# Kernel tuning notes

Hardware: AMD Instinct MI355X
Metric: run time of the kernel (lower is better)

## Reference

```python
import jax, jax.numpy as jnp
import numpy as np

B, IN, ED, PW, OUT, CL, NK = 2048, 4096, 8192, 2048, 256, 16, 32
MIX = 0.5

def _onehot_mask(key, n):
    # near-one-hot selector matrix [n, NK], as built by forward_update_masks
    idx = jax.random.choice(key, n, (NK,), replace=False)
    return jnp.zeros((n, NK), jnp.float32).at[idx, jnp.arange(NK)].set(1.0)

def setup_inputs():
    ks = jax.random.split(jax.random.key(0), 24)
    f = jnp.float32
    adj = (jax.random.uniform(ks[4], (IN, IN)) < 0.01).astype(f)
    adj = jnp.maximum(adj, adj.T).at[jnp.arange(IN), jnp.arange(IN)].set(1.0)
    return {
        'x_gene': jax.random.normal(ks[0], (B, IN), f),
        'x_invmea': jax.random.normal(ks[1], (B, IN), f),
        'x_curv': jax.random.normal(ks[2], (B, ED), f),
        'clinn': jax.random.normal(ks[3], (B, CL), f),
        'Adj': adj,
        'edge_mask': (jax.random.uniform(ks[5], (ED, IN)) < 0.005).astype(f),
        'pathway_mask': (jax.random.uniform(ks[6], (PW, ED)) < 0.02).astype(f),
        'top_gene_mask': _onehot_mask(ks[7], IN),
        'top_invmea_mask': _onehot_mask(ks[8], IN),
        'top_curv_mask': _onehot_mask(ks[9], ED),
        'top_path_mask': _onehot_mask(ks[10], PW),
        'W1': jnp.full((IN, IN), 0.05, f),
        'b1': 0.01 * jax.random.normal(ks[11], (IN,), f),
        'W2': jnp.full((ED, IN), 0.05, f),
        'b2': 0.01 * jax.random.normal(ks[12], (ED,), f),
        'W3': jnp.full((PW, ED), 0.05, f),
        'b3': 0.01 * jax.random.normal(ks[13], (PW,), f),
        'W4': 0.02 * jax.random.normal(ks[14], (OUT, PW), f),
        'b4': 0.01 * jax.random.normal(ks[15], (OUT,), f),
        'W5': 0.02 * jax.random.normal(ks[16], (OUT, OUT), f),
        'b5': 0.01 * jax.random.normal(ks[17], (OUT,), f),
        'W6': 0.05 * jax.random.normal(ks[18], (OUT, OUT + CL + 4 * NK), f),
        'W7': 0.05 * jax.random.normal(ks[19], (1, OUT), f),
        'mp11': MIX * jnp.ones(IN, f),
        'mp12': (1.0 - MIX) * jnp.ones(IN, f),
        'mp1': jnp.ones(IN, f),
        'mp21': MIX * jnp.ones(ED, f),
        'mp22': (1.0 - MIX) * jnp.ones(ED, f),
        'mp2': jnp.ones(ED, f),
        'mp3': jnp.ones(PW, f),
    }

def reference(x_gene, x_invmea, x_curv, clinn, Adj, edge_mask, pathway_mask,
              top_gene_mask, top_invmea_mask, top_curv_mask, top_path_mask,
              W1, b1, W2, b2, W3, b3, W4, b4, W5, b5, W6, W7,
              mp11, mp12, mp1, mp21, mp22, mp2, mp3):
    sg = jax.lax.stop_gradient
    sig = jax.nn.sigmoid
    kept_gene = sg(x_gene @ top_gene_mask)                     # [B,NK] gather-as-matmul
    x1 = sig(x_gene @ (W1 * Adj).T + b1)                       # masked linear [B,IN]
    x1 = x_invmea * (mp11 * mp1) + x1 * (mp12 * mp1)
    kept_invmea = sg(x1 @ top_invmea_mask)
    x1 = sig(x1 @ (W2 * edge_mask).T + b2)                     # [B,ED]
    x1 = x_curv * (mp21 * mp2) + x1 * (mp22 * mp2)
    kept_curv = sg(x1 @ top_curv_mask)
    x1 = sig(x1 @ (W3 * pathway_mask).T + b3)                  # [B,PW]
    x1 = x1 * mp3
    kept_path = sg(x1 @ top_path_mask)
    x1 = sig(x1 @ W4.T + b4)
    x1 = sig(x1 @ W5.T + b5)                                   # [B,OUT]
    x_cat = jnp.concatenate([x1, kept_gene, kept_invmea, kept_curv, kept_path, clinn], axis=1)
    lp = sig(x_cat @ W6.T)
    lp = lp - jnp.mean(lp, axis=1, keepdims=True)
    return lp @ W7.T                                           # [B,1]
```

## Files before the change

### kernel.cpp

```cpp
#include <hip/hip_runtime.h>

typedef unsigned short u16;
typedef __attribute__((ext_vector_type(4))) float f32x4;
typedef __attribute__((ext_vector_type(8))) short s16x8;

__device__ __forceinline__ u16 f2bf(float f) {
    union { float f; unsigned u; } c; c.f = f;
    return (u16)((c.u + 0x7fffu + ((c.u >> 16) & 1u)) >> 16);
}
__device__ __forceinline__ float bf2f(u16 u) {
    union { unsigned u; float f; } c; c.u = ((unsigned)u) << 16; return c.f;
}
__device__ __forceinline__ unsigned pk2(float a, float b) {
    return (unsigned)f2bf(a) | ((unsigned)f2bf(b) << 16);
}
__device__ __forceinline__ float sigm(float x) { return 1.0f / (1.0f + __expf(-x)); }
__device__ __forceinline__ void fma2(unsigned xv, float w, float& a0, float& a1) {
    union { float f; unsigned u; } lo, hi;
    lo.u = xv << 16; hi.u = xv & 0xFFFF0000u;
    a0 += w * lo.f; a1 += w * hi.f;
}

__device__ __forceinline__ void load16_g2l(const void* g, void* l) {
    __builtin_amdgcn_global_load_lds(
        (const __attribute__((address_space(1))) unsigned int*)(unsigned long long)g,
        (__attribute__((address_space(3))) unsigned int*)(unsigned int)(unsigned long long)l,
        16, 0, 0);
}

__device__ void d_transpF(const float* __restrict__ in, u16* __restrict__ out,
                          int Rr, int Cc, int bx, int by, float (*t)[65]) {
    const int r0 = by * 64, c0 = bx * 64;
    const int tid = threadIdx.x;
#pragma unroll
    for (int i = 0; i < 16; i++) {
        int idx = tid + i * 256;
        int rr = idx >> 6, cc = idx & 63;
        t[rr][cc] = in[(size_t)(r0 + rr) * Cc + c0 + cc];
    }
    __syncthreads();
#pragma unroll
    for (int i = 0; i < 16; i++) {
        int idx = tid + i * 256;
        int cc = idx >> 6, rr = idx & 63;
        out[(size_t)(c0 + cc) * Rr + r0 + rr] = f2bf(t[rr][cc]);
    }
}

__device__ void d_find(const float* __restrict__ mask, int n, int* __restrict__ outp,
                       int* red, int k) {
    int best = -1;
    for (int i = threadIdx.x; i < n; i += 256)
        if (mask[(size_t)i * 32 + k] != 0.0f) best = i;
    red[threadIdx.x] = best;
    __syncthreads();
    for (int off = 128; off > 0; off >>= 1) {
        if (threadIdx.x < off) {
            int o = red[threadIdx.x + off];
            if (o > red[threadIdx.x]) red[threadIdx.x] = o;
        }
        __syncthreads();
    }
    if (threadIdx.x == 0) *outp = red[0] < 0 ? 0 : red[0];
}

__device__ void d_conv(const float* __restrict__ in, u16* __restrict__ out,
                       int bid, unsigned n8) {
    unsigned i = bid * 256u + threadIdx.x;
    if (i >= n8) return;
    float4 a = ((const float4*)in)[2 * i];
    float4 b = ((const float4*)in)[2 * i + 1];
    uint4 o;
    o.x = pk2(a.x, a.y); o.y = pk2(a.z, a.w);
    o.z = pk2(b.x, b.y); o.w = pk2(b.z, b.w);
    ((uint4*)out)[i] = o;
}

__global__ __launch_bounds__(256) void prep_misc(
    const float* __restrict__ xg_f, const float* __restrict__ xinv_f,
    const float* __restrict__ xcv_f,
    u16* __restrict__ xTg, u16* __restrict__ xinvT, u16* __restrict__ xcvT,
    const float* __restrict__ m0, const float* __restrict__ m1,
    const float* __restrict__ m2, const float* __restrict__ m3,
    int* __restrict__ idx,
    const float* __restrict__ W4, u16* __restrict__ w4b,
    const float* __restrict__ W5, u16* __restrict__ w5b) {
    __shared__ float tile[64][65];
    int id = blockIdx.x;
    if (id < 2048) { d_transpF(xg_f, xTg, 2048, 4096, id & 63, id >> 6, tile); return; }
    id -= 2048;
    if (id < 2048) { d_transpF(xinv_f, xinvT, 2048, 4096, id & 63, id >> 6, tile); return; }
    id -= 2048;
    if (id < 4096) { d_transpF(xcv_f, xcvT, 2048, 8192, id & 127, id >> 7, tile); return; }
    id -= 4096;
    if (id < 128) {
        const float* mk; int n;
        int which = id >> 5;
        if (which == 0)      { mk = m0; n = 4096; }
        else if (which == 1) { mk = m1; n = 4096; }
        else if (which == 2) { mk = m2; n = 8192; }
        else                 { mk = m3; n = 2048; }
        d_find(mk, n, idx + which * 32 + (id & 31), (int*)tile, id & 31);
        return;
    }
    id -= 128;
    if (id < 256) { d_conv(W4, w4b, id, 65536u); return; }
    id -= 256;
    d_conv(W5, w5b, id, 8192u);
}

template <int CHUNKS>
__device__ void d_ell_reg(const float* __restrict__ M, const float* __restrict__ W,
                          unsigned* __restrict__ ell, int* __restrict__ cnt,
                          int PAD, int R, int bid) {
    const int lane = threadIdx.x & 63;
    const int row = bid * 4 + (threadIdx.x >> 6);
    if (row >= R) return;
    const int C = CHUNKS * 2048;
    const float4* mrow = (const float4*)(M + (size_t)row * C);
    const float4* wrow = (const float4*)(W + (size_t)row * C);
    unsigned* erow = ell + (size_t)row * PAD;
    int base = 0;
#pragma unroll
    for (int h = 0; h < CHUNKS; h++) {
        float4 m[8], w[8];
#pragma unroll
        for (int i = 0; i < 8; i++) m[i] = mrow[h * 512 + lane + i * 64];
#pragma unroll
        for (int i = 0; i < 8; i++) w[i] = wrow[h * 512 + lane + i * 64];
        int n = 0;
#pragma unroll
        for (int i = 0; i < 8; i++)
            n += (m[i].x != 0.f) + (m[i].y != 0.f) + (m[i].z != 0.f) + (m[i].w != 0.f);
        int pre = n;
#pragma unroll
        for (int off = 1; off < 64; off <<= 1) {
            int t = __shfl_up(pre, off, 64);
            if (lane >= off) pre += t;
        }
        int s = base + pre - n;
#pragma unroll
        for (int i = 0; i < 8; i++) {
            int c = h * 2048 + lane * 4 + i * 256;
            if (m[i].x != 0.f) { if (s < PAD) erow[s] = ((unsigned)f2bf(w[i].x) << 16) | (unsigned)(c + 0); s++; }
            if (m[i].y != 0.f) { if (s < PAD) erow[s] = ((unsigned)f2bf(w[i].y) << 16) | (unsigned)(c + 1); s++; }
            if (m[i].z != 0.f) { if (s < PAD) erow[s] = ((unsigned)f2bf(w[i].z) << 16) | (unsigned)(c + 2); s++; }
            if (m[i].w != 0.f) { if (s < PAD) erow[s] = ((unsigned)f2bf(w[i].w) << 16) | (unsigned)(c + 3); s++; }
        }
        base += __shfl(pre, 63, 64);
    }
    if (lane == 0) cnt[row] = base > PAD ? PAD : base;
}

__global__ __launch_bounds__(256) void prep_ell(
    const float* __restrict__ Adj, const float* __restrict__ W1,
    unsigned* __restrict__ ell1, int* __restrict__ cnt1,
    const float* __restrict__ edge, const float* __restrict__ W2,
    unsigned* __restrict__ ell2, int* __restrict__ cnt2,
    const float* __restrict__ path, const float* __restrict__ W3,
    unsigned* __restrict__ ell3, int* __restrict__ cnt3) {
    int id = blockIdx.x;
    if (id < 1024) { d_ell_reg<2>(Adj, W1, ell1, cnt1, 256, 4096, id); return; }
    id -= 1024;
    if (id < 2048) { d_ell_reg<2>(edge, W2, ell2, cnt2, 96, 8192, id); return; }
    id -= 2048;
    d_ell_reg<4>(path, W3, ell3, cnt3, 320, 2048, id);
}

template <int BPL>
__global__ __launch_bounds__(256) void spmm(const unsigned* __restrict__ ell,
                                            const int* __restrict__ cnt,
                                            const u16* __restrict__ xT,
                                            u16* __restrict__ outT,
                                            const float* __restrict__ bias,
                                            const float* __restrict__ c1a,
                                            const float* __restrict__ c1b,
                                            const float* __restrict__ c2a,
                                            const float* __restrict__ c2b,
                                            const u16* __restrict__ invT,
                                            const int* __restrict__ gidx,
                                            u16* __restrict__ gdst,
                                            int PAD) {
    const int lane = threadIdx.x & 63;
    const int wv = __builtin_amdgcn_readfirstlane((int)(threadIdx.x >> 6));
    const int j = blockIdx.y * 4 + wv;
    const int b0 = blockIdx.x * (64 * BPL) + lane * BPL;

    const unsigned* ep = ell + (size_t)j * PAD;
    int len = cnt[j];
    if (len > PAD) len = PAD;

    float acc[BPL];
#pragma unroll
    for (int i = 0; i < BPL; i++) acc[i] = 0.f;

    const int nfull = len >> 3;
    unsigned eA[8];
    if (nfull > 0) {
#pragma unroll
        for (int t = 0; t < 8; t++) eA[t] = ep[t];
    }
    for (int g = 0; g < nfull; g++) {
        unsigned eB[8];
        const bool more = (g + 1 < nfull);
        if (more) {
#pragma unroll
            for (int t = 0; t < 8; t++) eB[t] = ep[(g + 1) * 8 + t];
        }
        if (BPL == 8) {
            uint4 xv[8];
#pragma unroll
            for (int t = 0; t < 8; t++)
                xv[t] = *(const uint4*)(xT + ((size_t)(eA[t] & 0xFFFFu) << 11) + b0);
#pragma unroll
            for (int t = 0; t < 8; t++) {
                union { float f; unsigned u; } w; w.u = (eA[t] >> 16) << 16;
                fma2(xv[t].x, w.f, acc[0], acc[1]);
                fma2(xv[t].y, w.f, acc[2], acc[3]);
                fma2(xv[t].z, w.f, acc[4], acc[5]);
                fma2(xv[t].w, w.f, acc[6], acc[7]);
            }
        } else {
            uint2 xv[8];
#pragma unroll
            for (int t = 0; t < 8; t++)
                xv[t] = *(const uint2*)(xT + ((size_t)(eA[t] & 0xFFFFu) << 11) + b0);
#pragma unroll
            for (int t = 0; t < 8; t++) {
                union { float f; unsigned u; } w; w.u = (eA[t] >> 16) << 16;
                fma2(xv[t].x, w.f, acc[0], acc[1]);
                fma2(xv[t].y, w.f, acc[2], acc[3]);
            }
        }
        if (more) {
#pragma unroll
            for (int t = 0; t < 8; t++) eA[t] = eB[t];
        }
    }
    for (int s = nfull * 8; s < len; ++s) {
        unsigned e = ep[s];
        union { float f; unsigned u; } w; w.u = (e >> 16) << 16;
        const u16* xp = xT + ((size_t)(e & 0xFFFFu) << 11) + b0;
        if (BPL == 8) {
            uint4 xv = *(const uint4*)xp;
            fma2(xv.x, w.f, acc[0], acc[1]); fma2(xv.y, w.f, acc[2], acc[3]);
            fma2(xv.z, w.f, acc[4], acc[5]); fma2(xv.w, w.f, acc[6], acc[7]);
        } else {
            uint2 xv = *(const uint2*)xp;
            fma2(xv.x, w.f, acc[0], acc[1]); fma2(xv.y, w.f, acc[2], acc[3]);
        }
    }

    const float bi = bias[j];
    float c1 = 0.f;
    if (c1a) { c1 = c1a[j]; if (c1b) c1 *= c1b[j]; }
    float c2 = 1.f;
    if (c2a) { c2 = c2a[j]; if (c2b) c2 *= c2b[j]; }

    float v[BPL];
#pragma unroll
    for (int i = 0; i < BPL; i++) v[i] = sigm(acc[i] + bi) * c2;
    if (invT) {
        const unsigned long long* ip = (const unsigned long long*)(invT + ((size_t)j << 11) + b0);
#pragma unroll
        for (int h = 0; h < BPL / 4; h++) {
            unsigned long long iv = __builtin_nontemporal_load(ip + h);
            unsigned lo = (unsigned)iv, hi = (unsigned)(iv >> 32);
            union { float f; unsigned u; } g0, g1, g2, g3;
            g0.u = lo << 16; g1.u = lo & 0xFFFF0000u;
            g2.u = hi << 16; g3.u = hi & 0xFFFF0000u;
            v[4 * h + 0] += g0.f * c1; v[4 * h + 1] += g1.f * c1;
            v[4 * h + 2] += g2.f * c1; v[4 * h + 3] += g3.f * c1;
        }
    }
    unsigned long long pkv[BPL / 4];
#pragma unroll
    for (int h = 0; h < BPL / 4; h++)
        pkv[h] = (unsigned long long)pk2(v[4 * h + 0], v[4 * h + 1])
               | ((unsigned long long)pk2(v[4 * h + 2], v[4 * h + 3]) << 32);
    unsigned long long* op = (unsigned long long*)(outT + ((size_t)j << 11) + b0);
#pragma unroll
    for (int h = 0; h < BPL / 4; h++) __builtin_nontemporal_store(pkv[h], op + h);

    if (gdst) {
        for (int t = 0; t < 32; t++) {
            if (gidx[t] == j) {
                unsigned long long* gp = (unsigned long long*)(gdst + t * 2048 + b0);
#pragma unroll
                for (int h = 0; h < BPL / 4; h++) gp[h] = pkv[h];
            }
        }
    }
}

__global__ __launch_bounds__(256) void gatherFT(const float* __restrict__ src, int ld,
                                                const int* __restrict__ idx,
                                                u16* __restrict__ dstT) {
    int i = blockIdx.x * 256 + threadIdx.x;
    int kk = i >> 11, b = i & 2047;
    dstT[i] = f2bf(src[(size_t)b * ld + idx[kk]]);
}

__global__ __launch_bounds__(256) void transpB(const u16* __restrict__ in,
                                               u16* __restrict__ out, int Rr, int Cc) {
    __shared__ u16 t[64][66];
    const int r0 = blockIdx.y * 64, c0 = blockIdx.x * 64;
    const int tid = threadIdx.x;
#pragma unroll
    for (int i = 0; i < 16; i++) {
        int idx = tid + i * 256;
        int rr = idx >> 6, cc = idx & 63;
        t[rr][cc] = in[(size_t)(r0 + rr) * Cc + c0 + cc];
    }
    __syncthreads();
#pragma unroll
    for (int i = 0; i < 16; i++) {
        int idx = tid + i * 256;
        int cc = idx >> 6, rr = idx & 63;
        out[(size_t)(c0 + cc) * Rr + r0 + rr] = t[rr][cc];
    }
}

template <int WR, int WC, int MF, int NF, int KC, int WPE>
__global__ __launch_bounds__(WR * WC * 64, WPE)
void gemm_t(const u16* __restrict__ A, const u16* __restrict__ W,
            u16* __restrict__ Out, const float* __restrict__ bias, int N, int K) {
    constexpr int NTHR = WR * WC * 64;
    constexpr int BM = WR * MF * 16;
    constexpr int BN = WC * NF * 16;
    constexpr int BK = KC * 32;
    constexpr int CPR = KC * 4;
    constexpr int MSK = CPR - 1;
    constexpr int CA = BM * CPR / NTHR;
    constexpr int CB = BN * CPR / NTHR;
    constexpr int L  = CA + CB;

    __shared__ u16 At[2][BM * BK];
    __shared__ u16 Bt[2][BN * BK];

    const int tid = threadIdx.x;
    const int lane = tid & 63;
    const int wave = tid >> 6;
    const int wr = wave / WC, wc = wave % WC;
    const int tn = blockIdx.x, tm = blockIdx.y;
    const int r16 = lane & 15;
    const int q = lane >> 4;

    const u16* aSrc[CA]; int aDst[CA];
#pragma unroll
    for (int j = 0; j < CA; j++) {
        int c = tid + j * NTHR;
        int r = c / CPR, p = c - r * CPR;
        aSrc[j] = A + (size_t)(tm * BM + r) * K + (p ^ (r & MSK)) * 8;
        aDst[j] = c * 8;
    }
    const u16* bSrc[CB]; int bDst[CB];
#pragma unroll
    for (int j = 0; j < CB; j++) {
        int c = tid + j * NTHR;
        int r = c / CPR, p = c - r * CPR;
        bSrc[j] = W + (size_t)(tn * BN + r) * K + (p ^ (r & MSK)) * 8;
        bDst[j] = c * 8;
    }
    int aRd[MF][KC], bRd[NF][KC];
#pragma unroll
    for (int mi = 0; mi < MF; mi++)
#pragma unroll
        for (int kc = 0; kc < KC; kc++)
            aRd[mi][kc] = (wr * MF * 16 + mi * 16 + r16) * BK + (((kc * 4 + q) ^ (r16 & MSK)) << 3);
#pragma unroll
    for (int ni = 0; ni < NF; ni++)
#pragma unroll
        for (int kc = 0; kc < KC; kc++)
            bRd[ni][kc] = (wc * NF * 16 + ni * 16 + r16) * BK + (((kc * 4 + q) ^ (r16 & MSK)) << 3);

    const int nIter = K / BK;

#define ISSUE(slot, it_)                                              \
    do {                                                              \
        const int k0_ = (it_) * BK;                                   \
        _Pragma("unroll")                                             \
        for (int j = 0; j < CA; j++)                                  \
            load16_g2l(aSrc[j] + k0_, &At[slot][aDst[j]]);            \
        _Pragma("unroll")                                             \
        for (int j = 0; j < CB; j++)                                  \
            load16_g2l(bSrc[j] + k0_, &Bt[slot][bDst[j]]);            \
    } while (0)

    ISSUE(0, 0);
    if (nIter > 1) ISSUE(1, 1);

    f32x4 acc[MF][NF];
#pragma unroll
    for (int i = 0; i < MF; i++)
#pragma unroll
        for (int j = 0; j < NF; j++) acc[i][j] = (f32x4){0.f, 0.f, 0.f, 0.f};

    for (int it = 0; it < nIter; ++it) {
        const int s = it & 1;
        if (it + 1 < nIter) __builtin_amdgcn_s_waitcnt(0xF70 | L);
        else                __builtin_amdgcn_s_waitcnt(0xF70);
        __asm__ volatile("" ::: "memory");
        __builtin_amdgcn_s_barrier();
        __asm__ volatile("" ::: "memory");

        s16x8 af[KC][MF], bfr[KC][NF];
#pragma unroll
        for (int kc = 0; kc < KC; kc++) {
#pragma unroll
            for (int mi = 0; mi < MF; mi++) af[kc][mi] = *(const s16x8*)(&At[s][aRd[mi][kc]]);
#pragma unroll
            for (int ni = 0; ni < NF; ni++) bfr[kc][ni] = *(const s16x8*)(&Bt[s][bRd[ni][kc]]);
        }
        __asm__ volatile("" ::: "memory");
        __builtin_amdgcn_s_waitcnt(0xC07F);
        __builtin_amdgcn_s_barrier();
        __asm__ volatile("" ::: "memory");

        if (it + 2 < nIter) ISSUE(s, it + 2);

#pragma unroll
        for (int kc = 0; kc < KC; kc++)
#pragma unroll
            for (int mi = 0; mi < MF; mi++)
#pragma unroll
                for (int ni = 0; ni < NF; ni++)
                    acc[mi][ni] = __builtin_amdgcn_mfma_f32_16x16x32_bf16(af[kc][mi], bfr[kc][ni], acc[mi][ni], 0, 0, 0);
    }
#undef ISSUE

#pragma unroll
    for (int ni = 0; ni < NF; ni++) {
        const int n = tn * BN + wc * NF * 16 + ni * 16 + r16;
        const float bi = bias ? bias[n] : 0.f;
#pragma unroll
        for (int mi = 0; mi < MF; mi++) {
#pragma unroll
            for (int rg = 0; rg < 4; rg++) {
                const int m = tm * BM + wr * MF * 16 + mi * 16 + q * 4 + rg;
                Out[(size_t)m * N + n] = f2bf(sigm(acc[mi][ni][rg] + bi));
            }
        }
    }
}

__global__ __launch_bounds__(256) void tail_k(const u16* __restrict__ x5,
                                              const u16* __restrict__ kgT,
                                              const u16* __restrict__ kiT,
                                              const u16* __restrict__ kcT,
                                              const u16* __restrict__ kpT,
                                              const float* __restrict__ clinn,
                                              const float* __restrict__ W6,
                                              const float* __restrict__ W7,
                                              float* __restrict__ out) {
    __shared__ float xs[8 * 400];
    __shared__ float s1[4][8], s2[4][8], s3[4];
    const int tid = threadIdx.x;
    const int b0 = blockIdx.x * 8;
    for (int i = tid; i < 8 * 400; i += 256) {
        int r = i / 400, c = i - r * 400;
        int b = b0 + r;
        float v;
        if (c < 256)      v = bf2f(x5[b * 256 + c]);
        else if (c < 288) v = bf2f(kgT[(c - 256) * 2048 + b]);
        else if (c < 320) v = bf2f(kiT[(c - 288) * 2048 + b]);
        else if (c < 352) v = bf2f(kcT[(c - 320) * 2048 + b]);
        else if (c < 384) v = bf2f(kpT[(c - 352) * 2048 + b]);
        else              v = clinn[b * 16 + (c - 384)];
        xs[i] = v;
    }
    __syncthreads();
    const int j = tid;
    float acc[8];
#pragma unroll
    for (int r = 0; r < 8; r++) acc[r] = 0.f;
    const float4* wrow = (const float4*)(W6 + (size_t)j * 400);
    for (int c = 0; c < 100; c++) {
        float4 wv = wrow[c];
        const float* wp = (const float*)&wv;
#pragma unroll
        for (int t = 0; t < 4; t++) {
            float w = wp[t];
            int k = c * 4 + t;
#pragma unroll
            for (int r = 0; r < 8; r++) acc[r] += w * xs[r * 400 + k];
        }
    }
    const float w7j = W7[j];
    const int lane = tid & 63, wave = tid >> 6;
    float t3 = w7j;
#pragma unroll
    for (int off = 32; off > 0; off >>= 1) t3 += __shfl_down(t3, off, 64);
    if (lane == 0) s3[wave] = t3;
#pragma unroll
    for (int r = 0; r < 8; r++) {
        float lp = sigm(acc[r]);
        float t1 = lp, t2 = lp * w7j;
#pragma unroll
        for (int off = 32; off > 0; off >>= 1) {
            t1 += __shfl_down(t1, off, 64);
            t2 += __shfl_down(t2, off, 64);
        }
        if (lane == 0) { s1[wave][r] = t1; s2[wave][r] = t2; }
    }
    __syncthreads();
    if (tid < 8) {
        float S1 = s1[0][tid] + s1[1][tid] + s1[2][tid] + s1[3][tid];
        float S2 = s2[0][tid] + s2[1][tid] + s2[2][tid] + s2[3][tid];
        float SW = s3[0] + s3[1] + s3[2] + s3[3];
        out[b0 + tid] = S2 - (S1 * (1.f / 256.f)) * SW;
    }
}

extern "C" void kernel_launch(void* const* d_in, const int* in_sizes, int n_in,
                              void* d_out, int out_size, void* d_ws, size_t ws_size,
                              hipStream_t stream) {
    const float* x_gene   = (const float*)d_in[0];
    const float* x_invmea = (const float*)d_in[1];
    const float* x_curv   = (const float*)d_in[2];
    const float* clinn    = (const float*)d_in[3];
    const float* Adj      = (const float*)d_in[4];
    const float* edge_m   = (const float*)d_in[5];
    const float* path_m   = (const float*)d_in[6];
    const float* tg_mask  = (const float*)d_in[7];
    const float* ti_mask  = (const float*)d_in[8];
    const float* tc_mask  = (const float*)d_in[9];
    const float* tp_mask  = (const float*)d_in[10];
    const float* W1 = (const float*)d_in[11];  const float* b1 = (const float*)d_in[12];
    const float* W2 = (const float*)d_in[13];  const float* b2 = (const float*)d_in[14];
    const float* W3 = (const float*)d_in[15];  const float* b3 = (const float*)d_in[16];
    const float* W4 = (const float*)d_in[17];  const float* b4 = (const float*)d_in[18];
    const float* W5 = (const float*)d_in[19];  const float* b5 = (const float*)d_in[20];
    const float* W6 = (const float*)d_in[21];
    const float* W7 = (const float*)d_in[22];
    const float* mp11 = (const float*)d_in[23];
    const float* mp12 = (const float*)d_in[24];
    const float* mp1  = (const float*)d_in[25];
    const float* mp21 = (const float*)d_in[26];
    const float* mp22 = (const float*)d_in[27];
    const float* mp2  = (const float*)d_in[28];
    const float* mp3  = (const float*)d_in[29];

    char* ws = (char*)d_ws;
    const float* nulf = nullptr;
    float* out = (float*)d_out;

    u16*  xTg   = (u16*)(ws + 0);
    u16*  xinvT = (u16*)(ws + 16777216);
    u16*  xcvT  = (u16*)(ws + 33554432);
    u16*  x1T   = (u16*)(ws + 67108864);
    u16*  x2T   = (u16*)(ws + 83886080);
    u16*  x3T   = (u16*)(ws + 117440512);
    u16*  x3    = (u16*)(ws + 125829120);
    unsigned* ell1 = (unsigned*)(ws + 134217728);
    unsigned* ell2 = (unsigned*)(ws + 138412032);
    unsigned* ell3 = (unsigned*)(ws + 141557760);
    int* cnt1 = (int*)(ws + 144179200);
    int* cnt2 = (int*)(ws + 144195584);
    int* cnt3 = (int*)(ws + 144228352);
    int* idxg = (int*)(ws + 144236544);
    int* idxi = idxg + 32;
    int* idxc = idxg + 64;
    int* idxp = idxg + 96;
    u16* kgT  = (u16*)(ws + 144237056);
    u16* kiT  = (u16*)(ws + 144368128);
    u16* kcT  = (u16*)(ws + 144499200);
    u16* kpT  = (u16*)(ws + 144630272);
    u16* w4b  = (u16*)(ws + 144761344);
    u16* w5b  = (u16*)(ws + 145809920);
    u16* x4   = (u16*)(ws + 145940992);
    u16* x5   = (u16*)(ws + 146989568);

    prep_ell<<<3584, 256, 0, stream>>>(
        Adj, W1, ell1, cnt1, edge_m, W2, ell2, cnt2, path_m, W3, ell3, cnt3);
    prep_misc<<<8608, 256, 0, stream>>>(
        x_gene, x_invmea, x_curv, xTg, xinvT, xcvT,
        tg_mask, ti_mask, tc_mask, tp_mask, idxg, W4, w4b, W5, w5b);
    gatherFT<<<256, 256, 0, stream>>>(x_gene, 4096, idxg, kgT);

    spmm<4><<<dim3(8, 1024), 256, 0, stream>>>(ell1, cnt1, xTg, x1T, b1,
                                               mp11, mp1, mp12, mp1, xinvT,
                                               idxi, kiT, 256);
    spmm<4><<<dim3(8, 2048), 256, 0, stream>>>(ell2, cnt2, x1T, x2T, b2,
                                               mp21, mp2, mp22, mp2, xcvT,
                                               idxc, kcT, 96);
    spmm<4><<<dim3(8, 512), 256, 0, stream>>>(ell3, cnt3, x2T, x3T, b3,
                                              nulf, nulf, mp3, nulf, (const u16*)nullptr,
                                              idxp, kpT, 320);
    transpB<<<dim3(32, 32), 256, 0, stream>>>(x3T, x3, 2048, 2048);

    gemm_t<2, 2, 2, 2, 2, 4><<<dim3(4, 32), 256, 0, stream>>>(x3, w4b, x4, b4, 256, 2048);
    gemm_t<2, 2, 2, 2, 2, 4><<<dim3(4, 32), 256, 0, stream>>>(x4, w5b, x5, b5, 256, 256);

    tail_k<<<256, 256, 0, stream>>>(x5, kgT, kiT, kcT, kpT, clinn, W6, W7, out);
}
```

Before: 896.2 us.

## Merge ELL build and transposes into one kernel, load weights only where mask nonzero

Fuses the ELL-building and transpose/conversion prep kernels into a single launch, interleaving ELL blocks evenly among the transpose blocks so that different kinds of work run at the same time. The ELL builder now reads the mask first and loads each weight float4 only when its mask group has a nonzero entry. Because the masks are very sparse, this skips most of the dense W1/W2/W3 reads. The cost is more divergent control flow, and the savings depend on how sparse the masks are.

Result: faster. 871.8 us (-2.7%).

```diff
diff --git a/kernel.cpp b/kernel.cpp
--- a/kernel.cpp
+++ b/kernel.cpp
@@ -76,7 +76,67 @@
     ((uint4*)out)[i] = o;
 }
 
-__global__ __launch_bounds__(256) void prep_misc(
+template <int CHUNKS>
+__device__ void d_ell_reg(const float* __restrict__ M, const float* __restrict__ W,
+                          unsigned* __restrict__ ell, int* __restrict__ cnt,
+                          int PAD, int R, int bid) {
+    const int lane = threadIdx.x & 63;
+    const int row = bid * 4 + (threadIdx.x >> 6);
+    if (row >= R) return;
+    const int C = CHUNKS * 2048;
+    const float4* mrow = (const float4*)(M + (size_t)row * C);
+    const float4* wrow = (const float4*)(W + (size_t)row * C);
+    unsigned* erow = ell + (size_t)row * PAD;
+    int base = 0;
+#pragma unroll
+    for (int h = 0; h < CHUNKS; h++) {
+        float4 m[8];
+#pragma unroll
+        for (int i = 0; i < 8; i++) m[i] = mrow[h * 512 + lane + i * 64];
+        unsigned bits = 0;
+#pragma unroll
+        for (int i = 0; i < 8; i++) {
+            if (m[i].x != 0.f) bits |= 1u << (4 * i);
+            if (m[i].y != 0.f) bits |= 2u << (4 * i);
+            if (m[i].z != 0.f) bits |= 4u << (4 * i);
+            if (m[i].w != 0.f) bits |= 8u << (4 * i);
+        }
+        float4 w[8];
+#pragma unroll
+        for (int i = 0; i < 8; i++)
+            if ((bits >> (4 * i)) & 0xFu) w[i] = wrow[h * 512 + lane + i * 64];
+        __asm__ volatile("" ::: "memory");
+
+        const int n = __popc(bits);
+        int pre = n;
+#pragma unroll
+        for (int off = 1; off < 64; off <<= 1) {
+            int t = __shfl_up(pre, off, 64);
+            if (lane >= off) pre += t;
+        }
+        int s = base + pre - n;
+#pragma unroll
+        for (int i = 0; i < 8; i++) {
+            if ((bits >> (4 * i)) & 0xFu) {
+                int c = h * 2048 + lane * 4 + i * 256;
+                if (bits & (1u << (4 * i))) { if (s < PAD) erow[s] = ((unsigned)f2bf(w[i].x) << 16) | (unsigned)(c + 0); s++; }
+                if (bits & (2u << (4 * i))) { if (s < PAD) erow[s] = ((unsigned)f2bf(w[i].y) << 16) | (unsigned)(c + 1); s++; }
+                if (bits & (4u << (4 * i))) { if (s < PAD) erow[s] = ((unsigned)f2bf(w[i].z) << 16) | (unsigned)(c + 2); s++; }
+                if (bits & (8u << (4 * i))) { if (s < PAD) erow[s] = ((unsigned)f2bf(w[i].w) << 16) | (unsigned)(c + 3); s++; }
+            }
+        }
+        base += __shfl(pre, 63, 64);
+    }
+    if (lane == 0) cnt[row] = base > PAD ? PAD : base;
+}
+
+__global__ __launch_bounds__(256) void prep_all(
+    const float* __restrict__ Adj, const float* __restrict__ W1,
+    unsigned* __restrict__ ell1, int* __restrict__ cnt1,
+    const float* __restrict__ edge, const float* __restrict__ W2,
+    unsigned* __restrict__ ell2, int* __restrict__ cnt2,
+    const float* __restrict__ path, const float* __restrict__ W3,
+    unsigned* __restrict__ ell3, int* __restrict__ cnt3,
     const float* __restrict__ xg_f, const float* __restrict__ xinv_f,
     const float* __restrict__ xcv_f,
     u16* __restrict__ xTg, u16* __restrict__ xinvT, u16* __restrict__ xcvT,
@@ -86,7 +146,19 @@
     const float* __restrict__ W4, u16* __restrict__ w4b,
     const float* __restrict__ W5, u16* __restrict__ w5b) {
     __shared__ float tile[64][65];
-    int id = blockIdx.x;
+    const long long T = 12192, E = 3584;
+    const int b = blockIdx.x;
+    const int ea = (int)(((long long)b * E) / T);
+    const int eb = (int)(((long long)(b + 1) * E) / T);
+    if (eb > ea) {
+        int id = ea;
+        if (id < 1024) { d_ell_reg<2>(Adj, W1, ell1, cnt1, 256, 4096, id); return; }
+        id -= 1024;
+        if (id < 2048) { d_ell_reg<2>(edge, W2, ell2, cnt2, 96, 8192, id); return; }
+        d_ell_reg<4>(path, W3, ell3, cnt3, 320, 2048, id - 2048);
+        return;
+    }
+    int id = b - ea;
     if (id < 2048) { d_transpF(xg_f, xTg, 2048, 4096, id & 63, id >> 6, tile); return; }
     id -= 2048;
     if (id < 2048) { d_transpF(xinv_f, xinvT, 2048, 4096, id & 63, id >> 6, tile); return; }
@@ -107,64 +179,6 @@
     if (id < 256) { d_conv(W4, w4b, id, 65536u); return; }
     id -= 256;
     d_conv(W5, w5b, id, 8192u);
-}
-
-template <int CHUNKS>
-__device__ void d_ell_reg(const float* __restrict__ M, const float* __restrict__ W,
-                          unsigned* __restrict__ ell, int* __restrict__ cnt,
-                          int PAD, int R, int bid) {
-    const int lane = threadIdx.x & 63;
-    const int row = bid * 4 + (threadIdx.x >> 6);
-    if (row >= R) return;
-    const int C = CHUNKS * 2048;
-    const float4* mrow = (const float4*)(M + (size_t)row * C);
-    const float4* wrow = (const float4*)(W + (size_t)row * C);
-    unsigned* erow = ell + (size_t)row * PAD;
-    int base = 0;
-#pragma unroll
-    for (int h = 0; h < CHUNKS; h++) {
-        float4 m[8], w[8];
-#pragma unroll
-        for (int i = 0; i < 8; i++) m[i] = mrow[h * 512 + lane + i * 64];
-#pragma unroll
-        for (int i = 0; i < 8; i++) w[i] = wrow[h * 512 + lane + i * 64];
-        int n = 0;
-#pragma unroll
-        for (int i = 0; i < 8; i++)
-            n += (m[i].x != 0.f) + (m[i].y != 0.f) + (m[i].z != 0.f) + (m[i].w != 0.f);
-        int pre = n;
-#pragma unroll
-        for (int off = 1; off < 64; off <<= 1) {
-            int t = __shfl_up(pre, off, 64);
-            if (lane >= off) pre += t;
-        }
-        int s = base + pre - n;
-#pragma unroll
-        for (int i = 0; i < 8; i++) {
-            int c = h * 2048 + lane * 4 + i * 256;
-            if (m[i].x != 0.f) { if (s < PAD) erow[s] = ((unsigned)f2bf(w[i].x) << 16) | (unsigned)(c + 0); s++; }
-            if (m[i].y != 0.f) { if (s < PAD) erow[s] = ((unsigned)f2bf(w[i].y) << 16) | (unsigned)(c + 1); s++; }
-            if (m[i].z != 0.f) { if (s < PAD) erow[s] = ((unsigned)f2bf(w[i].z) << 16) | (unsigned)(c + 2); s++; }
-            if (m[i].w != 0.f) { if (s < PAD) erow[s] = ((unsigned)f2bf(w[i].w) << 16) | (unsigned)(c + 3); s++; }
-        }
-        base += __shfl(pre, 63, 64);
-    }
-    if (lane == 0) cnt[row] = base > PAD ? PAD : base;
-}
-
-__global__ __launch_bounds__(256) void prep_ell(
-    const float* __restrict__ Adj, const float* __restrict__ W1,
-    unsigned* __restrict__ ell1, int* __restrict__ cnt1,
-    const float* __restrict__ edge, const float* __restrict__ W2,
-    unsigned* __restrict__ ell2, int* __restrict__ cnt2,
-    const float* __restrict__ path, const float* __restrict__ W3,
-    unsigned* __restrict__ ell3, int* __restrict__ cnt3) {
-    int id = blockIdx.x;
-    if (id < 1024) { d_ell_reg<2>(Adj, W1, ell1, cnt1, 256, 4096, id); return; }
-    id -= 1024;
-    if (id < 2048) { d_ell_reg<2>(edge, W2, ell2, cnt2, 96, 8192, id); return; }
-    id -= 2048;
-    d_ell_reg<4>(path, W3, ell3, cnt3, 320, 2048, id);
 }
 
 template <int BPL>
@@ -571,9 +585,8 @@
     u16* x4   = (u16*)(ws + 145940992);
     u16* x5   = (u16*)(ws + 146989568);
 
-    prep_ell<<<3584, 256, 0, stream>>>(
-        Adj, W1, ell1, cnt1, edge_m, W2, ell2, cnt2, path_m, W3, ell3, cnt3);
-    prep_misc<<<8608, 256, 0, stream>>>(
+    prep_all<<<12192, 256, 0, stream>>>(
+        Adj, W1, ell1, cnt1, edge_m, W2, ell2, cnt2, path_m, W3, ell3, cnt3,
         x_gene, x_invmea, x_curv, xTg, xinvT, xcvT,
         tg_mask, ti_mask, tc_mask, tp_mask, idxg, W4, w4b, W5, w5b);
     gatherFT<<<256, 256, 0, stream>>>(x_gene, 4096, idxg, kgT);
```
